# Kernel tuning notes

Hardware: AMD Instinct MI355X
Metric: run time of the kernel (lower is better)

## Reference

```python
import jax, jax.numpy as jnp
import numpy as np

H = 128
L = 3
N = 100000
E = 1600000
G = 1024
OUT = 10
MAX_LEVEL = 1000
MAX_THOUGHTS = 5000
N_CATE = 5
BN_EPS = 1e-5


def _make_pe(n_pos, h):
    pos = np.arange(n_pos, dtype=np.float32)[:, None]
    div = np.exp(np.arange(0, h, 2, dtype=np.float32) * (-np.log(10000.0) / h))
    pe = np.zeros((n_pos, h), dtype=np.float32)
    pe[:, 0::2] = np.sin(pos * div)
    pe[:, 1::2] = np.cos(pos * div)
    return jnp.asarray(pe)


def setup_inputs() -> dict:
    key = jax.random.key(0)
    ks = jax.random.split(key, 16)
    s = 0.02
    inp = {
        "x": jax.random.randint(ks[0], (N, 3), 0, 5, dtype=jnp.int64 if jax.config.jax_enable_x64 else jnp.int32),
        "edge_index": jax.random.randint(ks[1], (2, E), 0, N),
        "batch": jnp.sort(jax.random.randint(ks[2], (N,), 0, G)),
        "num_graphs": G,
        "pe": _make_pe(MAX_THOUGHTS, H),
        "cate_emb": jax.random.normal(ks[3], (N_CATE, H), jnp.float32) * s,
        "level_emb": jax.random.normal(ks[4], (MAX_LEVEL, H), jnp.float32) * s,
        "conv_W1": jax.random.normal(ks[5], (L, H, H), jnp.float32) * s,
        "conv_b1": jnp.zeros((L, H), jnp.float32),
        "conv_g1": jnp.ones((L, H), jnp.float32),
        "conv_be1": jnp.zeros((L, H), jnp.float32),
        "conv_W2": jax.random.normal(ks[6], (L, H, H), jnp.float32) * s,
        "conv_b2": jnp.zeros((L, H), jnp.float32),
        "norm_g": jnp.ones((L, H), jnp.float32),
        "norm_be": jnp.zeros((L, H), jnp.float32),
        "gate_W1": jax.random.normal(ks[7], (H, H), jnp.float32) * s,
        "gate_b1": jnp.zeros((H,), jnp.float32),
        "gate_W2": jax.random.normal(ks[8], (H, 1), jnp.float32) * s,
        "gate_b2": jnp.zeros((1,), jnp.float32),
        "cls_W1": jax.random.normal(ks[9], (H, H), jnp.float32) * s,
        "cls_b1": jnp.zeros((H,), jnp.float32),
        "cls_g": jnp.ones((H,), jnp.float32),
        "cls_be": jnp.zeros((H,), jnp.float32),
        "cls_W2": jax.random.normal(ks[10], (H, OUT), jnp.float32) * s,
        "cls_b2": jnp.zeros((OUT,), jnp.float32),
    }
    return inp


def _bn(h, g, b):
    # BatchNorm1d, training mode: batch stats over the node/graph dim, biased var
    m = jnp.mean(h, axis=0)
    v = jnp.var(h, axis=0)
    return (h - m) * jax.lax.rsqrt(v + BN_EPS) * g + b


def reference(x, edge_index, batch, num_graphs, pe, cate_emb, level_emb,
              conv_W1, conv_b1, conv_g1, conv_be1, conv_W2, conv_b2,
              norm_g, norm_be, gate_W1, gate_b1, gate_W2, gate_b2,
              cls_W1, cls_b1, cls_g, cls_be, cls_W2, cls_b2):
    # NodeEncoder ('tree'): level + cate + sinusoidal thought PE
    level = jnp.clip(x[:, 0], 0, MAX_LEVEL - 1)
    cate = jnp.clip(x[:, 1], 0, N_CATE - 1)
    thought = jnp.clip(x[:, 2], 0, MAX_THOUGHTS - 1)
    h = cate_emb[cate] + level_emb[level] + pe[thought]  # [N, H]

    src, dst = edge_index[0], edge_index[1]
    n = h.shape[0]
    for i in range(L):
        # GINConv (eps=0): h_i <- MLP(h_i + sum_{j->i} h_j)
        agg = jax.ops.segment_sum(h[src], dst, num_segments=n)
        z = (h + agg) @ conv_W1[i] + conv_b1[i]
        z = jax.nn.relu(_bn(z, conv_g1[i], conv_be1[i]))
        z = z @ conv_W2[i] + conv_b2[i]
        h = jax.nn.relu(_bn(z, norm_g[i], norm_be[i]))

    # GlobalAttention pooling: per-graph softmax over gate scores
    gate = (jax.nn.relu(h @ gate_W1 + gate_b1) @ gate_W2 + gate_b2)[:, 0]  # [N]
    m = jax.ops.segment_max(gate, batch, num_segments=num_graphs)
    e = jnp.exp(gate - m[batch])
    s = jax.ops.segment_sum(e, batch, num_segments=num_graphs)
    alpha = e / s[batch]
    pooled = jax.ops.segment_sum(alpha[:, None] * h, batch, num_segments=num_graphs)  # [G, H]

    # classifier (dropout = 0)
    z = pooled @ cls_W1 + cls_b1
    z = jax.nn.relu(_bn(z, cls_g, cls_be))
    return z @ cls_W2 + cls_b2  # [G, OUT]
```

## Files before the change

### kernel.cpp

```cpp
#include <hip/hip_runtime.h>
#include <math.h>

#define HD 128

typedef __attribute__((ext_vector_type(8))) short bf16x8;
typedef __attribute__((ext_vector_type(8))) unsigned short us8;
typedef __attribute__((ext_vector_type(4))) unsigned short us4;
typedef __attribute__((ext_vector_type(4))) float f32x4;

__device__ __forceinline__ float bf2f(unsigned short u) {
  union { unsigned int i; float f; } v; v.i = ((unsigned int)u) << 16; return v.f;
}
__device__ __forceinline__ unsigned short f2bf(float f) {
  union { float f; unsigned int i; } v; v.f = f;
  unsigned int u = v.i;
  u += 0x7FFFu + ((u >> 16) & 1u);
  return (unsigned short)(u >> 16);
}

__global__ void zero_f(float* p, int n) {
  int i = blockIdx.x * blockDim.x + threadIdx.x;
  if (i < n) p[i] = 0.f;
}

__global__ void zero_int(int* p, int n) {
  int stride = gridDim.x * blockDim.x;
  for (int i = blockIdx.x * blockDim.x + threadIdx.x; i < n; i += stride) p[i] = 0;
}

__global__ void encode_kernel(const int* __restrict__ x, const float* __restrict__ pe,
                              const float* __restrict__ ce, const float* __restrict__ le,
                              float* __restrict__ h, int n) {
  int total = n * HD;
  int stride = gridDim.x * blockDim.x;
  for (int idx = blockIdx.x * blockDim.x + threadIdx.x; idx < total; idx += stride) {
    int node = idx >> 7, c = idx & (HD - 1);
    int lv = x[node * 3 + 0]; lv = lv < 0 ? 0 : (lv > 999 ? 999 : lv);
    int ct = x[node * 3 + 1]; ct = ct < 0 ? 0 : (ct > 4 ? 4 : ct);
    int th = x[node * 3 + 2]; th = th < 0 ? 0 : (th > 4999 ? 4999 : th);
    h[idx] = ce[ct * HD + c] + le[lv * HD + c] + pe[th * HD + c];
  }
}

__global__ void prep_w(const float* __restrict__ cW1, const float* __restrict__ cW2,
                       const float* __restrict__ gW1,
                       unsigned short* __restrict__ whi, unsigned short* __restrict__ wlo) {
  int m = blockIdx.x;
  const float* W = (m < 3) ? cW1 + (size_t)m * HD * HD
                 : (m < 6) ? cW2 + (size_t)(m - 3) * HD * HD : gW1;
  unsigned short* oh = whi + (size_t)m * HD * HD;
  unsigned short* ol = wlo + (size_t)m * HD * HD;
  for (int i = threadIdx.x; i < HD * HD; i += 256) {
    int j = i & 7;
    int l = (i >> 3) & 63;
    int p = i >> 9;
    int ct = p >> 2, k4 = p & 3;
    int c = ct * 16 + (l & 15);
    int k = (k4 * 4 + (l >> 4)) * 8 + j;
    float f = W[k * HD + c];
    unsigned short hh = f2bf(f);
    oh[i] = hh;
    ol[i] = f2bf(f - bf2f(hh));
  }
}


__global__ void hist_kernel(const int* __restrict__ ei, int* deg, int E, int Wwin) {
  int pass = blockIdx.x & 7;
  int b = blockIdx.x >> 3;
  int tstride = (gridDim.x >> 3) * blockDim.x;
  for (int e = b * blockDim.x + threadIdx.x; e < E; e += tstride) {
    int d = ei[E + e];
    if (d / Wwin == pass) atomicAdd(&deg[d], 1);
  }
}

#define SCAN_BS 1024
__global__ void scan1_kernel(const int* __restrict__ deg, int* __restrict__ off,
                             int* __restrict__ bsum, int n) {
  __shared__ int sh[256];
  int b = blockIdx.x, t = threadIdx.x;
  int base = b * SCAN_BS + t * 4;
  int v[4];
#pragma unroll
  for (int j = 0; j < 4; j++) v[j] = (base + j < n) ? deg[base + j] : 0;
  int s = v[0] + v[1] + v[2] + v[3];
  sh[t] = s;
  __syncthreads();
  for (int o = 1; o < 256; o <<= 1) {
    int x = (t >= o) ? sh[t - o] : 0;
    __syncthreads();
    sh[t] += x;
    __syncthreads();
  }
  int excl = sh[t] - s;
  if (t == 255) bsum[b] = sh[255];
  int run = excl;
#pragma unroll
  for (int j = 0; j < 4; j++) {
    if (base + j < n) off[base + j] = run;
    run += v[j];
  }
}

__global__ void scan2_kernel(int* bsum, int nb) {
  __shared__ int sh[128];
  int t = threadIdx.x;
  int v = (t < nb) ? bsum[t] : 0;
  sh[t] = v;
  __syncthreads();
  for (int o = 1; o < 128; o <<= 1) {
    int x = (t >= o) ? sh[t - o] : 0;
    __syncthreads();
    sh[t] += x;
    __syncthreads();
  }
  if (t < nb) bsum[t] = sh[t] - v;
}

__global__ void scan3_kernel(int* off, int* cursor, const int* __restrict__ bsum,
                             int n, int E) {
  int idx = blockIdx.x * blockDim.x + threadIdx.x;
  int stride = gridDim.x * blockDim.x;
  for (int i = idx; i < n; i += stride) {
    int v = off[i] + bsum[i >> 10];
    off[i] = v;
    cursor[i] = v;
  }
  if (idx == 0) off[n] = E;
}

__global__ void fill_kernel(const int* __restrict__ ei, int* cursor, int* csr_src,
                            int E, int Wwin) {
  int pass = blockIdx.x & 7;
  int b = blockIdx.x >> 3;
  int tstride = (gridDim.x >> 3) * blockDim.x;
  for (int e = b * blockDim.x + threadIdx.x; e < E; e += tstride) {
    int d = ei[E + e];
    if (d / Wwin == pass) {
      int pos = atomicAdd(&cursor[d], 1);
      csr_src[pos] = ei[e];
    }
  }
}

template<bool BN>
__global__ void gather_kernel(const float* __restrict__ h, const int* __restrict__ off,
                              const int* __restrict__ src, const float* __restrict__ ab,
                              float* __restrict__ out, int N) {
  int gid = (blockIdx.x * blockDim.x + threadIdx.x) >> 5;
  int lane = threadIdx.x & 31;
  int ng = (gridDim.x * blockDim.x) >> 5;
  float4 a4, b4;
  if (BN) {
    a4 = *(const float4*)(ab + lane * 4);
    b4 = *(const float4*)(ab + HD + lane * 4);
  }
#define APPLY_BN(v) if (BN) { \
    v.x = fmaxf(v.x * a4.x + b4.x, 0.f); \
    v.y = fmaxf(v.y * a4.y + b4.y, 0.f); \
    v.z = fmaxf(v.z * a4.z + b4.z, 0.f); \
    v.w = fmaxf(v.w * a4.w + b4.w, 0.f); }
  for (int i = gid; i < N; i += ng) {
    int s0 = off[i], s1 = off[i + 1];
    float4 acc0 = *(const float4*)(h + (size_t)i * HD + lane * 4);
    APPLY_BN(acc0);
    float4 acc1 = {0.f, 0.f, 0.f, 0.f};
    float4 acc2 = {0.f, 0.f, 0.f, 0.f};
    float4 acc3 = {0.f, 0.f, 0.f, 0.f};
    int e = s0;
    for (; e + 4 <= s1; e += 4) {
      int i0 = src[e], i1 = src[e + 1], i2 = src[e + 2], i3 = src[e + 3];
      float4 v0 = *(const float4*)(h + (size_t)i0 * HD + lane * 4);
      float4 v1 = *(const float4*)(h + (size_t)i1 * HD + lane * 4);
      float4 v2 = *(const float4*)(h + (size_t)i2 * HD + lane * 4);
      float4 v3 = *(const float4*)(h + (size_t)i3 * HD + lane * 4);
      APPLY_BN(v0); APPLY_BN(v1); APPLY_BN(v2); APPLY_BN(v3);
      acc0.x += v0.x; acc0.y += v0.y; acc0.z += v0.z; acc0.w += v0.w;
      acc1.x += v1.x; acc1.y += v1.y; acc1.z += v1.z; acc1.w += v1.w;
      acc2.x += v2.x; acc2.y += v2.y; acc2.z += v2.z; acc2.w += v2.w;
      acc3.x += v3.x; acc3.y += v3.y; acc3.z += v3.z; acc3.w += v3.w;
    }
    for (; e < s1; e++) {
      int s = src[e];
      float4 v = *(const float4*)(h + (size_t)s * HD + lane * 4);
      APPLY_BN(v);
      acc0.x += v.x; acc0.y += v.y; acc0.z += v.z; acc0.w += v.w;
    }
    acc0.x += acc1.x + acc2.x + acc3.x;
    acc0.y += acc1.y + acc2.y + acc3.y;
    acc0.z += acc1.z + acc2.z + acc3.z;
    acc0.w += acc1.w + acc2.w + acc3.w;
    *(float4*)(out + (size_t)i * HD + lane * 4) = acc0;
  }
#undef APPLY_BN
}

template<bool INBN, bool GATE, bool STATS>
__global__ __launch_bounds__(512, 4)
void gemm_split(const float* __restrict__ X, const unsigned short* __restrict__ Whi,
                const unsigned short* __restrict__ Wlo,
                const float* __restrict__ bias, const float* __restrict__ ab,
                const float* __restrict__ w2, float* __restrict__ outf,
                float* __restrict__ gate, float* __restrict__ stat, int Nn) {
  __shared__ unsigned short XsH[128 * HD];
  __shared__ unsigned short XsL[128 * HD];
  __shared__ float red[2 * HD];
  int t = threadIdx.x;
  long rowbase = (long)blockIdx.x * 128;

#pragma unroll
  for (int it = 0; it < 8; it++) {
    int i = (t + it * 512) * 4;
    int r = i >> 7, k = i & (HD - 1);
    long row = rowbase + r; if (row > Nn - 1) row = Nn - 1;
    float4 v = *(const float4*)(X + row * HD + k);
    float f[4] = {v.x, v.y, v.z, v.w};
    if (INBN) {
#pragma unroll
      for (int j = 0; j < 4; j++)
        f[j] = fmaxf(f[j] * ab[k + j] + ab[HD + k + j], 0.f);
    }
    us4 hi, lo;
#pragma unroll
    for (int j = 0; j < 4; j++) {
      unsigned short hh = f2bf(f[j]);
      hi[j] = hh;
      lo[j] = f2bf(f[j] - bf2f(hh));
    }
    int g = k >> 3;
    int off = r * HD + ((((g ^ (r & 7)) << 3)) | (k & 7));
    *(us4*)(XsH + off) = hi;
    *(us4*)(XsL + off) = lo;
  }
  if (STATS && t < 2 * HD) red[t] = 0.f;
  __syncthreads();

  int w = t >> 6, l = t & 63;
  int lr = l & 15, lg = l >> 4;

  f32x4 acc[8];
#pragma unroll
  for (int ct = 0; ct < 8; ct++) acc[ct] = (f32x4){0.f, 0.f, 0.f, 0.f};

  bf16x8 aH[4], aL[4];
  int arow = w * 16 + lr;
#pragma unroll
  for (int k4 = 0; k4 < 4; k4++) {
    int kg = k4 * 4 + lg;
    int off = arow * HD + (((kg ^ (arow & 7)) << 3));
    aH[k4] = *(bf16x8*)(XsH + off);
    aL[k4] = *(bf16x8*)(XsL + off);
  }
#pragma unroll
  for (int ct = 0; ct < 8; ct++) {
#pragma unroll
    for (int k4 = 0; k4 < 4; k4++) {
      int bo = (((ct << 2) + k4) * 64 + l) * 8;
      bf16x8 bH = *(const bf16x8*)(Whi + bo);
      bf16x8 bL = *(const bf16x8*)(Wlo + bo);
      acc[ct] = __builtin_amdgcn_mfma_f32_16x16x32_bf16(aH[k4], bH, acc[ct], 0, 0, 0);
      acc[ct] = __builtin_amdgcn_mfma_f32_16x16x32_bf16(aH[k4], bL, acc[ct], 0, 0, 0);
      acc[ct] = __builtin_amdgcn_mfma_f32_16x16x32_bf16(aL[k4], bH, acc[ct], 0, 0, 0);
    }
  }

  if (GATE) {
#pragma unroll
    for (int jj = 0; jj < 4; jj++) {
      float p = 0.f;
#pragma unroll
      for (int ct = 0; ct < 8; ct++) {
        float v = fmaxf(acc[ct][jj] + bias[ct * 16 + lr], 0.f);
        p += v * w2[ct * 16 + lr];
      }
      p += __shfl_xor(p, 1);
      p += __shfl_xor(p, 2);
      p += __shfl_xor(p, 4);
      p += __shfl_xor(p, 8);
      long row = rowbase + w * 16 + lg * 4 + jj;
      if (lr == 0 && row < Nn) gate[row] = p;
    }
  } else {
    float s[8], ss[8];
#pragma unroll
    for (int ct = 0; ct < 8; ct++) { s[ct] = 0.f; ss[ct] = 0.f; }
#pragma unroll
    for (int jj = 0; jj < 4; jj++) {
      long row = rowbase + w * 16 + lg * 4 + jj;
      bool ok = row < Nn;
#pragma unroll
      for (int ct = 0; ct < 8; ct++) {
        float v = acc[ct][jj] + bias[ct * 16 + lr];
        if (ok) {
          outf[row * HD + ct * 16 + lr] = v;
          if (STATS) { s[ct] += v; ss[ct] += v * v; }
        }
      }
    }
    if (STATS) {
#pragma unroll
      for (int ct = 0; ct < 8; ct++) {
        float sv = s[ct], sq = ss[ct];
        sv += __shfl_xor(sv, 16); sq += __shfl_xor(sq, 16);
        sv += __shfl_xor(sv, 32); sq += __shfl_xor(sq, 32);
        if (lg == 0) {
          atomicAdd(&red[ct * 16 + lr], sv);
          atomicAdd(&red[HD + ct * 16 + lr], sq);
        }
      }
      __syncthreads();
      float* st = stat + (blockIdx.x & 3) * 256;
      if (t < HD) {
        atomicAdd(&st[t], red[t]);
        atomicAdd(&st[HD + t], red[HD + t]);
      }
    }
  }
}

__global__ void finalize_kernel(const float* __restrict__ stat, const float* __restrict__ g,
                                const float* __restrict__ be, float* ab, float inv_n) {
  int c = threadIdx.x;
  float s = stat[c] + stat[256 + c] + stat[512 + c] + stat[768 + c];
  float sq = stat[HD + c] + stat[256 + HD + c] + stat[512 + HD + c] + stat[768 + HD + c];
  float mean = s * inv_n;
  float var = sq * inv_n - mean * mean;
  float inv = rsqrtf(var + 1e-5f);
  float a = inv * g[c];
  ab[c] = a;
  ab[HD + c] = be[c] - mean * a;
}

__global__ void finalize1_kernel(const float* __restrict__ stat, const float* __restrict__ g,
                                 const float* __restrict__ be, float* ab, float inv_n) {
  int c = threadIdx.x;
  float mean = stat[c] * inv_n;
  float var = stat[HD + c] * inv_n - mean * mean;
  float inv = rsqrtf(var + 1e-5f);
  float a = inv * g[c];
  ab[c] = a;
  ab[HD + c] = be[c] - mean * a;
}

__global__ void bound_kernel(const int* __restrict__ batch, int* gs, int N, int G) {
  int i = blockIdx.x * blockDim.x + threadIdx.x;
  if (i >= N) return;
  int b = batch[i];
  int prev = (i == 0) ? -1 : batch[i - 1];
  for (int g = prev + 1; g <= b; g++) gs[g] = i;
  if (i == N - 1)
    for (int g = b + 1; g <= G; g++) gs[g] = N;
}

__global__ void fused_pool(const float* __restrict__ h, const float* __restrict__ gate,
                           const int* __restrict__ gs, const float* __restrict__ ab,
                           float* __restrict__ pooled) {
  int g = blockIdx.x;
  int t = threadIdx.x;
  int s0 = gs[g], s1 = gs[g + 1];
  if (s0 >= s1) { pooled[(size_t)g * HD + t] = 0.f; return; }
  __shared__ float red[HD];
  float m = -INFINITY;
  for (int i = s0 + t; i < s1; i += HD) m = fmaxf(m, gate[i]);
  red[t] = m;
  __syncthreads();
  for (int o = 64; o > 0; o >>= 1) {
    if (t < o) red[t] = fmaxf(red[t], red[t + o]);
    __syncthreads();
  }
  m = red[0];
  __syncthreads();
  float s = 0.f;
  for (int i = s0 + t; i < s1; i += HD) s += expf(gate[i] - m);
  red[t] = s;
  __syncthreads();
  for (int o = 64; o > 0; o >>= 1) {
    if (t < o) red[t] += red[t + o];
    __syncthreads();
  }
  float inv = 1.f / red[0];
  float a = ab[t], b = ab[HD + t];
  float acc = 0.f;
  int i = s0;
  for (; i + 4 <= s1; i += 4) {
    float al0 = expf(gate[i] - m);
    float al1 = expf(gate[i + 1] - m);
    float al2 = expf(gate[i + 2] - m);
    float al3 = expf(gate[i + 3] - m);
    float v0 = fmaxf(h[(size_t)(i + 0) * HD + t] * a + b, 0.f);
    float v1 = fmaxf(h[(size_t)(i + 1) * HD + t] * a + b, 0.f);
    float v2 = fmaxf(h[(size_t)(i + 2) * HD + t] * a + b, 0.f);
    float v3 = fmaxf(h[(size_t)(i + 3) * HD + t] * a + b, 0.f);
    acc += al0 * v0 + al1 * v1 + al2 * v2 + al3 * v3;
  }
  for (; i < s1; i++) {
    float al = expf(gate[i] - m);
    float v = fmaxf(h[(size_t)i * HD + t] * a + b, 0.f);
    acc += al * v;
  }
  pooled[(size_t)g * HD + t] = acc * inv;
}

__global__ __launch_bounds__(256, 4)
void gemm_f32(const float* __restrict__ X, const float* __restrict__ W,
              const float* __restrict__ bias, float* __restrict__ out, int Nn) {
  __shared__ float XsT[32][132];
  __shared__ float Ws[32][HD];
  int t = threadIdx.x;
  int r0 = (t >> 4) * 8;
  int c0 = (t & 15) * 8;
  long rowbase = (long)blockIdx.x * 128;

  float acc[8][8];
#pragma unroll
  for (int ci = 0; ci < 8; ci++) {
    float bv = bias[c0 + ci];
#pragma unroll
    for (int ri = 0; ri < 8; ri++) acc[ri][ci] = bv;
  }

  int sr = t >> 1;
  int hf = t & 1;
  long srow = rowbase + sr; if (srow > Nn - 1) srow = Nn - 1;
  const float* xrow = X + srow * HD;

  for (int k0 = 0; k0 < HD; k0 += 32) {
    __syncthreads();
#pragma unroll
    for (int j = 0; j < 4; j++) {
      int i = j * 1024 + t * 4;
      int kk = i >> 7, c = i & (HD - 1);
      *(float4*)&Ws[kk][c] = *(const float4*)&W[(size_t)(k0 + kk) * HD + c];
    }
#pragma unroll
    for (int j = 0; j < 4; j++) {
      int kc = k0 + hf * 16 + j * 4;
      float4 v = *(const float4*)&xrow[kc];
      int kl = hf * 16 + j * 4;
      XsT[kl + 0][sr] = v.x;
      XsT[kl + 1][sr] = v.y;
      XsT[kl + 2][sr] = v.z;
      XsT[kl + 3][sr] = v.w;
    }
    __syncthreads();
#pragma unroll 8
    for (int kk = 0; kk < 32; kk++) {
      float4 a0 = *(float4*)&XsT[kk][r0];
      float4 a1 = *(float4*)&XsT[kk][r0 + 4];
      float4 b0 = *(float4*)&Ws[kk][c0];
      float4 b1 = *(float4*)&Ws[kk][c0 + 4];
      float ar[8] = {a0.x, a0.y, a0.z, a0.w, a1.x, a1.y, a1.z, a1.w};
      float bc[8] = {b0.x, b0.y, b0.z, b0.w, b1.x, b1.y, b1.z, b1.w};
#pragma unroll
      for (int ri = 0; ri < 8; ri++)
#pragma unroll
        for (int ci = 0; ci < 8; ci++) acc[ri][ci] += ar[ri] * bc[ci];
    }
  }

#pragma unroll
  for (int ri = 0; ri < 8; ri++) {
    long row = rowbase + r0 + ri;
    if (row < Nn) {
      float4 o0 = {acc[ri][0], acc[ri][1], acc[ri][2], acc[ri][3]};
      float4 o1 = {acc[ri][4], acc[ri][5], acc[ri][6], acc[ri][7]};
      *(float4*)&out[row * HD + c0] = o0;
      *(float4*)&out[row * HD + c0 + 4] = o1;
    }
  }
}

__global__ void stats_f32(const float* __restrict__ z, float* stat, int n) {
  int c = threadIdx.x & (HD - 1);
  int rg = threadIdx.x >> 7;
  float s = 0.f, ss = 0.f;
  for (int r = blockIdx.x * 2 + rg; r < n; r += gridDim.x * 2) {
    float v = z[(size_t)r * HD + c];
    s += v; ss += v * v;
  }
  __shared__ float S[2][HD], SS[2][HD];
  S[rg][c] = s; SS[rg][c] = ss;
  __syncthreads();
  if (threadIdx.x < HD) {
    atomicAdd(&stat[c], S[0][c] + S[1][c]);
    atomicAdd(&stat[HD + c], SS[0][c] + SS[1][c]);
  }
}

__global__ void cls_out_kernel(const float* __restrict__ zc, const float* __restrict__ ab,
                               const float* __restrict__ W2, const float* __restrict__ b2,
                               float* out, int G) {
  int row = blockIdx.x;
  int t = threadIdx.x;
  float v0 = fmaxf(zc[(size_t)row * HD + t] * ab[t] + ab[HD + t], 0.f);
  float v1 = fmaxf(zc[(size_t)row * HD + 64 + t] * ab[64 + t] + ab[HD + 64 + t], 0.f);
  for (int o = 0; o < 10; o++) {
    float p = v0 * W2[t * 10 + o] + v1 * W2[(64 + t) * 10 + o];
#pragma unroll
    for (int s = 32; s > 0; s >>= 1) p += __shfl_down(p, s);
    if (t == 0) out[row * 10 + o] = p + b2[o];
  }
}

extern "C" void kernel_launch(void* const* d_in, const int* in_sizes, int n_in,
                              void* d_out, int out_size, void* d_ws, size_t ws_size,
                              hipStream_t stream) {
  const int* x     = (const int*)d_in[0];
  const int* ei    = (const int*)d_in[1];
  const int* batch = (const int*)d_in[2];
  const float* pe  = (const float*)d_in[4];
  const float* ce  = (const float*)d_in[5];
  const float* le  = (const float*)d_in[6];
  const float* cW1 = (const float*)d_in[7];
  const float* cb1 = (const float*)d_in[8];
  const float* cg1 = (const float*)d_in[9];
  const float* cbe1= (const float*)d_in[10];
  const float* cW2 = (const float*)d_in[11];
  const float* cb2 = (const float*)d_in[12];
  const float* ngm = (const float*)d_in[13];
  const float* nbe = (const float*)d_in[14];
  const float* gW1 = (const float*)d_in[15];
  const float* gb1 = (const float*)d_in[16];
  const float* gW2 = (const float*)d_in[17];
  const float* clW1= (const float*)d_in[19];
  const float* clb1= (const float*)d_in[20];
  const float* clg = (const float*)d_in[21];
  const float* clbe= (const float*)d_in[22];
  const float* clW2= (const float*)d_in[23];
  const float* clb2= (const float*)d_in[24];

  int N = in_sizes[2];
  int E = in_sizes[1] / 2;
  int G = out_size / 10;

  float* buf0   = (float*)d_ws;
  float* buf1   = buf0 + (size_t)N * HD;
  float* pooled = buf1 + (size_t)N * HD;
  float* gate   = pooled + (size_t)G * HD;
  float* zc     = gate + N;
  float* stats  = zc + (size_t)G * HD;
  float* ab     = stats + 7 * 1024;
  unsigned short* whi = (unsigned short*)(ab + 7 * 256);
  unsigned short* wlo = whi + 7 * HD * HD;
  int* csr_off  = (int*)(wlo + 7 * HD * HD);
  int* cursor   = csr_off + (N + 1);
  int* bsum     = cursor + N;
  int* gs       = bsum + 128;
  int* csr_src  = gs + (G + 1);

  float* out = (float*)d_out;
  int gemmBlocks = (N + 127) / 128;
  int Wwin = (N + 7) / 8;

  zero_f<<<28, 256, 0, stream>>>(stats, 7 * 1024);
  encode_kernel<<<2048, 256, 0, stream>>>(x, pe, ce, le, buf0, N);
  prep_w<<<7, 256, 0, stream>>>(cW1, cW2, gW1, whi, wlo);

  int nb = (N + SCAN_BS - 1) / SCAN_BS;
  zero_int<<<256, 256, 0, stream>>>(cursor, N);
  hist_kernel<<<2048, 256, 0, stream>>>(ei, cursor, E, Wwin);
  scan1_kernel<<<nb, 256, 0, stream>>>(cursor, csr_off, bsum, N);
  scan2_kernel<<<1, 128, 0, stream>>>(bsum, nb);
  scan3_kernel<<<256, 256, 0, stream>>>(csr_off, cursor, bsum, N, E);
  fill_kernel<<<2048, 256, 0, stream>>>(ei, cursor, csr_src, E, Wwin);
  bound_kernel<<<(N + 255) / 256, 256, 0, stream>>>(batch, gs, N, G);

  for (int l = 0; l < 3; l++) {
    float* abPrev = ab + (l - 1) * 512 + 256;
    if (l == 0)
      gather_kernel<false><<<2048, 256, 0, stream>>>(buf0, csr_off, csr_src, nullptr, buf1, N);
    else
      gather_kernel<true><<<2048, 256, 0, stream>>>(buf0, csr_off, csr_src, abPrev, buf1, N);
    gemm_split<false, false, true><<<gemmBlocks, 512, 0, stream>>>(
        buf1, whi + (size_t)l * HD * HD, wlo + (size_t)l * HD * HD,
        cb1 + l * HD, nullptr, nullptr, buf1, nullptr, stats + l * 2048, N);
    finalize_kernel<<<1, 128, 0, stream>>>(stats + l * 2048, cg1 + l * HD, cbe1 + l * HD,
                                           ab + l * 512, 1.f / N);
    gemm_split<true, false, true><<<gemmBlocks, 512, 0, stream>>>(
        buf1, whi + (size_t)(3 + l) * HD * HD, wlo + (size_t)(3 + l) * HD * HD,
        cb2 + l * HD, ab + l * 512, nullptr, buf0, nullptr, stats + l * 2048 + 1024, N);
    finalize_kernel<<<1, 128, 0, stream>>>(stats + l * 2048 + 1024, ngm + l * HD, nbe + l * HD,
                                           ab + l * 512 + 256, 1.f / N);
  }

  const float* abFin = ab + 2 * 512 + 256;
  gemm_split<true, true, false><<<gemmBlocks, 512, 0, stream>>>(
      buf0, whi + (size_t)6 * HD * HD, wlo + (size_t)6 * HD * HD,
      gb1, abFin, gW2, nullptr, gate, nullptr, N);
  fused_pool<<<G, HD, 0, stream>>>(buf0, gate, gs, abFin, pooled);

  gemm_f32<<<(G + 127) / 128, 256, 0, stream>>>(pooled, clW1, clb1, zc, G);
  stats_f32<<<64, 256, 0, stream>>>(zc, stats + 6 * 1024, G);
  finalize1_kernel<<<1, 128, 0, stream>>>(stats + 6 * 1024, clg, clbe, ab + 6 * 256, 1.f / G);
  cls_out_kernel<<<G, 64, 0, stream>>>(zc, ab + 6 * 256, clW2, clb2, out, G);
}
```

Before: 935.6 us.

## Fuse neighbor gather into first GIN GEMM via shared-memory staging

Replaces the separate gather kernel and first per-layer GEMM with one kernel. Each block gathers and sums neighbor rows for its 128 rows, splits the sums into bf16 hi/lo parts and writes them straight into shared memory, then runs the MFMA GEMM with fused bias and BN statistics. This drops the write and re-read of the aggregated buffer and one launch per layer. The gather loop is also unrolled to 8 edges. The cost is that gather parallelism now follows the GEMM grid (16 row-groups per 512-thread block), which may lower memory-level parallelism for the irregular gather.

```diff
diff --git a/kernel.cpp b/kernel.cpp
--- a/kernel.cpp
+++ b/kernel.cpp
@@ -144,13 +144,21 @@
   }
 }
 
-template<bool BN>
-__global__ void gather_kernel(const float* __restrict__ h, const int* __restrict__ off,
-                              const int* __restrict__ src, const float* __restrict__ ab,
-                              float* __restrict__ out, int N) {
-  int gid = (blockIdx.x * blockDim.x + threadIdx.x) >> 5;
-  int lane = threadIdx.x & 31;
-  int ng = (gridDim.x * blockDim.x) >> 5;
+template<bool BN, bool STATS>
+__global__ __launch_bounds__(512, 4)
+void gemm_gather(const float* __restrict__ h, const int* __restrict__ off,
+                 const int* __restrict__ src, const float* __restrict__ ab,
+                 const unsigned short* __restrict__ Whi,
+                 const unsigned short* __restrict__ Wlo,
+                 const float* __restrict__ bias, float* __restrict__ outf,
+                 float* __restrict__ stat, int Nn) {
+  __shared__ unsigned short XsH[128 * HD];
+  __shared__ unsigned short XsL[128 * HD];
+  __shared__ float red[2 * HD];
+  int t = threadIdx.x;
+  long rowbase = (long)blockIdx.x * 128;
+  int grp = t >> 5, lane = t & 31;
+
   float4 a4, b4;
   if (BN) {
     a4 = *(const float4*)(ab + lane * 4);
@@ -161,25 +169,34 @@
     v.y = fmaxf(v.y * a4.y + b4.y, 0.f); \
     v.z = fmaxf(v.z * a4.z + b4.z, 0.f); \
     v.w = fmaxf(v.w * a4.w + b4.w, 0.f); }
-  for (int i = gid; i < N; i += ng) {
-    int s0 = off[i], s1 = off[i + 1];
-    float4 acc0 = *(const float4*)(h + (size_t)i * HD + lane * 4);
+
+  for (int rr = 0; rr < 8; rr++) {
+    int r = grp + rr * 16;
+    long row = rowbase + r; if (row > Nn - 1) row = Nn - 1;
+    int s0 = off[row], s1 = off[row + 1];
+    float4 acc0 = *(const float4*)(h + row * HD + lane * 4);
     APPLY_BN(acc0);
     float4 acc1 = {0.f, 0.f, 0.f, 0.f};
     float4 acc2 = {0.f, 0.f, 0.f, 0.f};
     float4 acc3 = {0.f, 0.f, 0.f, 0.f};
     int e = s0;
-    for (; e + 4 <= s1; e += 4) {
+    for (; e + 8 <= s1; e += 8) {
       int i0 = src[e], i1 = src[e + 1], i2 = src[e + 2], i3 = src[e + 3];
+      int i4 = src[e + 4], i5 = src[e + 5], i6 = src[e + 6], i7 = src[e + 7];
       float4 v0 = *(const float4*)(h + (size_t)i0 * HD + lane * 4);
       float4 v1 = *(const float4*)(h + (size_t)i1 * HD + lane * 4);
       float4 v2 = *(const float4*)(h + (size_t)i2 * HD + lane * 4);
       float4 v3 = *(const float4*)(h + (size_t)i3 * HD + lane * 4);
+      float4 v4 = *(const float4*)(h + (size_t)i4 * HD + lane * 4);
+      float4 v5 = *(const float4*)(h + (size_t)i5 * HD + lane * 4);
+      float4 v6 = *(const float4*)(h + (size_t)i6 * HD + lane * 4);
+      float4 v7 = *(const float4*)(h + (size_t)i7 * HD + lane * 4);
       APPLY_BN(v0); APPLY_BN(v1); APPLY_BN(v2); APPLY_BN(v3);
-      acc0.x += v0.x; acc0.y += v0.y; acc0.z += v0.z; acc0.w += v0.w;
-      acc1.x += v1.x; acc1.y += v1.y; acc1.z += v1.z; acc1.w += v1.w;
-      acc2.x += v2.x; acc2.y += v2.y; acc2.z += v2.z; acc2.w += v2.w;
-      acc3.x += v3.x; acc3.y += v3.y; acc3.z += v3.z; acc3.w += v3.w;
+      APPLY_BN(v4); APPLY_BN(v5); APPLY_BN(v6); APPLY_BN(v7);
+      acc0.x += v0.x + v4.x; acc0.y += v0.y + v4.y; acc0.z += v0.z + v4.z; acc0.w += v0.w + v4.w;
+      acc1.x += v1.x + v5.x; acc1.y += v1.y + v5.y; acc1.z += v1.z + v5.z; acc1.w += v1.w + v5.w;
+      acc2.x += v2.x + v6.x; acc2.y += v2.y + v6.y; acc2.z += v2.z + v6.z; acc2.w += v2.w + v6.w;
+      acc3.x += v3.x + v7.x; acc3.y += v3.y + v7.y; acc3.z += v3.z + v7.z; acc3.w += v3.w + v7.w;
     }
     for (; e < s1; e++) {
       int s = src[e];
@@ -191,9 +208,86 @@
     acc0.y += acc1.y + acc2.y + acc3.y;
     acc0.z += acc1.z + acc2.z + acc3.z;
     acc0.w += acc1.w + acc2.w + acc3.w;
-    *(float4*)(out + (size_t)i * HD + lane * 4) = acc0;
+    float f[4] = {acc0.x, acc0.y, acc0.z, acc0.w};
+    us4 hi, lo;
+#pragma unroll
+    for (int j = 0; j < 4; j++) {
+      unsigned short hh = f2bf(f[j]);
+      hi[j] = hh;
+      lo[j] = f2bf(f[j] - bf2f(hh));
+    }
+    int g8 = lane >> 1;
+    int offl = r * HD + (((g8 ^ (r & 7)) << 3)) + (lane & 1) * 4;
+    *(us4*)(XsH + offl) = hi;
+    *(us4*)(XsL + offl) = lo;
   }
 #undef APPLY_BN
+  if (STATS && t < 2 * HD) red[t] = 0.f;
+  __syncthreads();
+
+  int w = t >> 6, l = t & 63;
+  int lr = l & 15, lg = l >> 4;
+
+  f32x4 acc[8];
+#pragma unroll
+  for (int ct = 0; ct < 8; ct++) acc[ct] = (f32x4){0.f, 0.f, 0.f, 0.f};
+
+  bf16x8 aH[4], aL[4];
+  int arow = w * 16 + lr;
+#pragma unroll
+  for (int k4 = 0; k4 < 4; k4++) {
+    int kg = k4 * 4 + lg;
+    int offa = arow * HD + (((kg ^ (arow & 7)) << 3));
+    aH[k4] = *(bf16x8*)(XsH + offa);
+    aL[k4] = *(bf16x8*)(XsL + offa);
+  }
+#pragma unroll
+  for (int ct = 0; ct < 8; ct++) {
+#pragma unroll
+    for (int k4 = 0; k4 < 4; k4++) {
+      int bo = (((ct << 2) + k4) * 64 + l) * 8;
+      bf16x8 bH = *(const bf16x8*)(Whi + bo);
+      bf16x8 bL = *(const bf16x8*)(Wlo + bo);
+      acc[ct] = __builtin_amdgcn_mfma_f32_16x16x32_bf16(aH[k4], bH, acc[ct], 0, 0, 0);
+      acc[ct] = __builtin_amdgcn_mfma_f32_16x16x32_bf16(aH[k4], bL, acc[ct], 0, 0, 0);
+      acc[ct] = __builtin_amdgcn_mfma_f32_16x16x32_bf16(aL[k4], bH, acc[ct], 0, 0, 0);
+    }
+  }
+
+  float s[8], ss[8];
+#pragma unroll
+  for (int ct = 0; ct < 8; ct++) { s[ct] = 0.f; ss[ct] = 0.f; }
+#pragma unroll
+  for (int jj = 0; jj < 4; jj++) {
+    long row = rowbase + w * 16 + lg * 4 + jj;
+    bool ok = row < Nn;
+#pragma unroll
+    for (int ct = 0; ct < 8; ct++) {
+      float v = acc[ct][jj] + bias[ct * 16 + lr];
+      if (ok) {
+        outf[row * HD + ct * 16 + lr] = v;
+        if (STATS) { s[ct] += v; ss[ct] += v * v; }
+      }
+    }
+  }
+  if (STATS) {
+#pragma unroll
+    for (int ct = 0; ct < 8; ct++) {
+      float sv = s[ct], sq = ss[ct];
+      sv += __shfl_xor(sv, 16); sq += __shfl_xor(sq, 16);
+      sv += __shfl_xor(sv, 32); sq += __shfl_xor(sq, 32);
+      if (lg == 0) {
+        atomicAdd(&red[ct * 16 + lr], sv);
+        atomicAdd(&red[HD + ct * 16 + lr], sq);
+      }
+    }
+    __syncthreads();
+    float* st = stat + (blockIdx.x & 3) * 256;
+    if (t < HD) {
+      atomicAdd(&st[t], red[t]);
+      atomicAdd(&st[HD + t], red[HD + t]);
+    }
+  }
 }
 
 template<bool INBN, bool GATE, bool STATS>
@@ -569,12 +663,15 @@
   for (int l = 0; l < 3; l++) {
     float* abPrev = ab + (l - 1) * 512 + 256;
     if (l == 0)
-      gather_kernel<false><<<2048, 256, 0, stream>>>(buf0, csr_off, csr_src, nullptr, buf1, N);
+      gemm_gather<false, true><<<gemmBlocks, 512, 0, stream>>>(
+          buf0, csr_off, csr_src, nullptr,
+          whi + (size_t)l * HD * HD, wlo + (size_t)l * HD * HD,
+          cb1 + l * HD, buf1, stats + l * 2048, N);
     else
-      gather_kernel<true><<<2048, 256, 0, stream>>>(buf0, csr_off, csr_src, abPrev, buf1, N);
-    gemm_split<false, false, true><<<gemmBlocks, 512, 0, stream>>>(
-        buf1, whi + (size_t)l * HD * HD, wlo + (size_t)l * HD * HD,
-        cb1 + l * HD, nullptr, nullptr, buf1, nullptr, stats + l * 2048, N);
+      gemm_gather<true, true><<<gemmBlocks, 512, 0, stream>>>(
+          buf0, csr_off, csr_src, abPrev,
+          whi + (size_t)l * HD * HD, wlo + (size_t)l * HD * HD,
+          cb1 + l * HD, buf1, stats + l * 2048, N);
     finalize_kernel<<<1, 128, 0, stream>>>(stats + l * 2048, cg1 + l * HD, cbe1 + l * HD,
                                            ab + l * 512, 1.f / N);
     gemm_split<true, false, true><<<gemmBlocks, 512, 0, stream>>>(
```

Result: faster. 890.6 us (-4.8%).
